# Optimization experiments

Hardware: AMD Instinct MI355X
Metric: run time of the kernel (lower is better)

## Reference

```python
import jax, jax.numpy as jnp
import numpy as np

DIM = 512
N_HEADS = 8
HEAD_DIM = DIM // N_HEADS
TOP_K_RATIO = 0.25
B, L = 2, 2048


def setup_inputs() -> dict:
    key = jax.random.key(0)
    k1, k2, k3, k4, k5 = jax.random.split(key, 5)
    s = 0.02
    return {
        "x": jax.random.normal(k1, (B, L, DIM), jnp.float32),
        "w_qkv": jax.random.normal(k2, (3 * DIM, DIM), jnp.float32) * s,
        "b_qkv": jnp.zeros((3 * DIM,), jnp.float32),
        "w_out": jax.random.normal(k3, (DIM, DIM), jnp.float32) * s,
        "b_out": jnp.zeros((DIM,), jnp.float32),
    }


def reference(x, w_qkv, b_qkv, w_out, b_out):
    Bx, Lx, C = x.shape
    scale = HEAD_DIM ** -0.5
    top_k = max(1, int(TOP_K_RATIO * Lx))

    qkv = x @ w_qkv.T + b_qkv  # [B, L, 3*C]
    qkv = qkv.reshape(Bx, Lx, 3, N_HEADS, HEAD_DIM)
    q, k, v = qkv[:, :, 0], qkv[:, :, 1], qkv[:, :, 2]  # [B, L, H, D]

    scores = jnp.einsum('blhd,bshd->bhls', q, k) * scale  # [B, H, L, L]

    _, top_idx = jax.lax.top_k(scores, top_k)  # [B, H, L, K]
    bi = jnp.arange(Bx)[:, None, None, None]
    hi = jnp.arange(N_HEADS)[None, :, None, None]
    li = jnp.arange(Lx)[None, None, :, None]
    mask = jnp.zeros(scores.shape, bool).at[bi, hi, li, top_idx].set(True)

    masked = jnp.where(mask, scores, -jnp.inf)
    probs = jax.nn.softmax(masked, axis=-1)  # [B, H, L, L]

    out = jnp.einsum('bhls,bshd->blhd', probs, v).reshape(Bx, Lx, C)
    return out @ w_out.T + b_out
```

## Files before the change

kernel.cpp:

```cpp
#include <hip/hip_runtime.h>

#define B_ 2
#define L_ 2048
#define DIM_ 512
#define NH_ 8
#define HD_ 64
#define TOPK_ 512

typedef __attribute__((ext_vector_type(8))) short short8;
typedef __attribute__((ext_vector_type(4))) float f32x4;
typedef unsigned short ushort_t;

__device__ __forceinline__ unsigned f2ord(float f) {
  unsigned u = __float_as_uint(f);
  return (u >> 31) ? ~u : (u | 0x80000000u);
}
__device__ __forceinline__ float ord2f(unsigned k) {
  unsigned u = (k >> 31) ? (k ^ 0x80000000u) : ~k;
  return __uint_as_float(u);
}
__device__ __forceinline__ ushort_t bfrne(float f) {
  unsigned u = __float_as_uint(f);
  return (ushort_t)((u + 0x7FFFu + ((u >> 16) & 1u)) >> 16);
}

__global__ __launch_bounds__(256) void gemm_qkv(
    const float* __restrict__ A, const float* __restrict__ Bw,
    const float* __restrict__ bias,
    ushort_t* __restrict__ Qh, ushort_t* __restrict__ Ql,
    ushort_t* __restrict__ Kh, ushort_t* __restrict__ Kl,
    ushort_t* __restrict__ Vt)
{
  constexpr int BM = 128, BN = 128, BK = 16, TM = 8, TN = 8;
  const int M = B_ * L_, N = 3 * DIM_, K = DIM_;
  __shared__ float As[BK][BM];
  __shared__ float Bs[BK][BN];
  const int tid = threadIdx.x;
  const int m0 = blockIdx.y * BM;
  const int n0 = blockIdx.x * BN;
  constexpr int TX = BN / TN;
  const int tn = (tid % TX) * TN;
  const int tm = (tid / TX) * TM;

  float acc[TM][TN];
#pragma unroll
  for (int i = 0; i < TM; ++i)
#pragma unroll
    for (int j = 0; j < TN; ++j) acc[i][j] = 0.f;

  constexpr int A4 = BM * BK / 4;
  constexpr int B4 = BN * BK / 4;

  for (int k0 = 0; k0 < K; k0 += BK) {
    for (int idx = tid; idx < A4; idx += 256) {
      int e = idx * 4;
      int row = e / BK, col = e % BK;
      float4 v = *(const float4*)(A + (size_t)(m0 + row) * K + k0 + col);
      As[col][row] = v.x; As[col+1][row] = v.y; As[col+2][row] = v.z; As[col+3][row] = v.w;
    }
    for (int idx = tid; idx < B4; idx += 256) {
      int e = idx * 4;
      int row = e / BK, col = e % BK;
      float4 v = *(const float4*)(Bw + (size_t)(n0 + row) * K + k0 + col);
      Bs[col][row] = v.x; Bs[col+1][row] = v.y; Bs[col+2][row] = v.z; Bs[col+3][row] = v.w;
    }
    __syncthreads();
#pragma unroll
    for (int kk = 0; kk < BK; ++kk) {
      float a[TM], b[TN];
#pragma unroll
      for (int i = 0; i < TM; i += 4) *(float4*)&a[i] = *(const float4*)&As[kk][tm + i];
#pragma unroll
      for (int j = 0; j < TN; j += 4) *(float4*)&b[j] = *(const float4*)&Bs[kk][tn + j];
#pragma unroll
      for (int i = 0; i < TM; ++i)
#pragma unroll
        for (int j = 0; j < TN; ++j) acc[i][j] = fmaf(a[i], b[j], acc[i][j]);
    }
    __syncthreads();
  }

#pragma unroll
  for (int i = 0; i < TM; ++i) {
    const int m = m0 + tm + i;
    const int b = m >> 11, l = m & (L_ - 1);
#pragma unroll
    for (int j = 0; j < TN; ++j) {
      const int n = n0 + tn + j;
      float v = acc[i][j] + bias[n];
      const int which = n >> 9, h = (n >> 6) & (NH_ - 1), d = n & (HD_ - 1);
      const int bh = b * NH_ + h;
      if (which == 0) {
        v *= 0.125f;
        ushort_t hi = bfrne(v);
        float hf = __uint_as_float((unsigned)hi << 16);
        ushort_t lo = bfrne(v - hf);
        const size_t o = ((size_t)bh * L_ + l) * HD_ + d;
        Qh[o] = hi; Ql[o] = lo;
      } else if (which == 1) {
        ushort_t hi = bfrne(v);
        float hf = __uint_as_float((unsigned)hi << 16);
        ushort_t lo = bfrne(v - hf);
        const size_t o = ((size_t)bh * L_ + l) * HD_ + d;
        Kh[o] = hi; Kl[o] = lo;
      } else {
        Vt[((size_t)bh * HD_ + d) * L_ + l] = bfrne(v);
      }
    }
  }
}

__global__ __launch_bounds__(256) void gemm_out(
    const float* __restrict__ A, const float* __restrict__ Bw,
    const float* __restrict__ bias, float* __restrict__ out)
{
  constexpr int BM = 64, BN = 64, BK = 16, TM = 4, TN = 4;
  const int N = DIM_, K = DIM_;
  __shared__ float As[BK][BM];
  __shared__ float Bs[BK][BN];
  const int tid = threadIdx.x;
  const int m0 = blockIdx.y * BM;
  const int n0 = blockIdx.x * BN;
  constexpr int TX = BN / TN;
  const int tn = (tid % TX) * TN;
  const int tm = (tid / TX) * TM;

  float acc[TM][TN];
#pragma unroll
  for (int i = 0; i < TM; ++i)
#pragma unroll
    for (int j = 0; j < TN; ++j) acc[i][j] = 0.f;

  constexpr int A4 = BM * BK / 4;
  constexpr int B4 = BN * BK / 4;

  for (int k0 = 0; k0 < K; k0 += BK) {
    for (int idx = tid; idx < A4; idx += 256) {
      int e = idx * 4;
      int row = e / BK, col = e % BK;
      float4 v = *(const float4*)(A + (size_t)(m0 + row) * K + k0 + col);
      As[col][row] = v.x; As[col+1][row] = v.y; As[col+2][row] = v.z; As[col+3][row] = v.w;
    }
    for (int idx = tid; idx < B4; idx += 256) {
      int e = idx * 4;
      int row = e / BK, col = e % BK;
      float4 v = *(const float4*)(Bw + (size_t)(n0 + row) * K + k0 + col);
      Bs[col][row] = v.x; Bs[col+1][row] = v.y; Bs[col+2][row] = v.z; Bs[col+3][row] = v.w;
    }
    __syncthreads();
#pragma unroll
    for (int kk = 0; kk < BK; ++kk) {
      float a[TM], b[TN];
#pragma unroll
      for (int i = 0; i < TM; i += 4) *(float4*)&a[i] = *(const float4*)&As[kk][tm + i];
#pragma unroll
      for (int j = 0; j < TN; j += 4) *(float4*)&b[j] = *(const float4*)&Bs[kk][tn + j];
#pragma unroll
      for (int i = 0; i < TM; ++i)
#pragma unroll
        for (int j = 0; j < TN; ++j) acc[i][j] = fmaf(a[i], b[j], acc[i][j]);
    }
    __syncthreads();
  }

#pragma unroll
  for (int i = 0; i < TM; ++i) {
    const int m = m0 + tm + i;
#pragma unroll
    for (int j = 0; j < TN; ++j)
      out[(size_t)m * N + n0 + tn + j] = acc[i][j] + bias[n0 + tn + j];
  }
}

__global__ __launch_bounds__(256, 4) void sgemm_k(
    const ushort_t* __restrict__ Qh, const ushort_t* __restrict__ Ql,
    const ushort_t* __restrict__ Kh, const ushort_t* __restrict__ Kl,
    float* __restrict__ S, int row0, int CH)
{
  const int lane = threadIdx.x & 63, wid = threadIdx.x >> 6;
  const int bh = blockIdx.z;
  const int m0 = blockIdx.y * 64;
  const int n0 = blockIdx.x * 128 + wid * 32;
  const int arow = lane & 15, agrp = lane >> 4;

  short8 kh[2][2], kl[2][2];
#pragma unroll
  for (int kt = 0; kt < 2; ++kt) {
    const size_t ka = ((size_t)bh * L_ + n0 + kt * 16 + arow) * HD_ + agrp * 8;
    kh[kt][0] = *(const short8*)(Kh + ka);
    kh[kt][1] = *(const short8*)(Kh + ka + 32);
    kl[kt][0] = *(const short8*)(Kl + ka);
    kl[kt][1] = *(const short8*)(Kl + ka + 32);
  }

  float* schunk = S + (size_t)bh * CH * L_;
#pragma unroll
  for (int rt = 0; rt < 4; ++rt) {
    const size_t qa = ((size_t)bh * L_ + row0 + m0 + rt * 16 + arow) * HD_ + agrp * 8;
    const short8 qh0 = *(const short8*)(Qh + qa);
    const short8 qh1 = *(const short8*)(Qh + qa + 32);
    const short8 ql0 = *(const short8*)(Ql + qa);
    const short8 ql1 = *(const short8*)(Ql + qa + 32);
#pragma unroll
    for (int kt = 0; kt < 2; ++kt) {
      f32x4 aA = {0.f, 0.f, 0.f, 0.f}, aB = {0.f, 0.f, 0.f, 0.f};
      aA = __builtin_amdgcn_mfma_f32_16x16x32_bf16(qh0, kh[kt][0], aA, 0, 0, 0);
      aB = __builtin_amdgcn_mfma_f32_16x16x32_bf16(qh1, kh[kt][1], aB, 0, 0, 0);
      aA = __builtin_amdgcn_mfma_f32_16x16x32_bf16(ql0, kh[kt][0], aA, 0, 0, 0);
      aB = __builtin_amdgcn_mfma_f32_16x16x32_bf16(ql1, kh[kt][1], aB, 0, 0, 0);
      aA = __builtin_amdgcn_mfma_f32_16x16x32_bf16(qh0, kl[kt][0], aA, 0, 0, 0);
      aB = __builtin_amdgcn_mfma_f32_16x16x32_bf16(qh1, kl[kt][1], aB, 0, 0, 0);
#pragma unroll
      for (int rr = 0; rr < 4; ++rr)
        schunk[(size_t)(m0 + rt * 16 + agrp * 4 + rr) * L_ + n0 + kt * 16 + arow]
            = aA[rr] + aB[rr];
    }
  }
}

__global__ __launch_bounds__(512, 4) void selpv_k(
    const float* __restrict__ S, const ushort_t* __restrict__ Vt,
    float* __restrict__ AO, int row0, int CH)
{
  __shared__ ushort_t pl[8][2056];
  __shared__ float red[8 * 512];
  __shared__ float invs[8];

  const int tid = threadIdx.x, lane = tid & 63, wid = tid >> 6;
  const int bh = blockIdx.y;
  const int blk = blockIdx.x;
  const int arow = lane & 15, agrp = lane >> 4;

  {
    const float* srow = S + ((size_t)bh * CH + blk * 8 + wid) * L_;
    unsigned keys[32];
    float mx = -3.0e38f;
#pragma unroll
    for (int t = 0; t < 32; ++t) {
      const float s = srow[lane + 64 * t];
      keys[t] = f2ord(s);
      mx = fmaxf(mx, s);
    }
#pragma unroll
    for (int off = 32; off; off >>= 1) mx = fmaxf(mx, __shfl_xor(mx, off));

    unsigned P = 0;
#pragma unroll 1
    for (int bit = 31; bit >= 8; --bit) {
      const unsigned cand = P | (1u << bit);
      int c = 0;
#pragma unroll
      for (int t = 0; t < 32; ++t)
        c += (int)__popcll(__ballot(keys[t] >= cand));
      if (c >= TOPK_) P = cand;
    }

    int base = 0;
    float part = 0.f;
#pragma unroll
    for (int t = 0; t < 32; ++t) {
      const bool sel = keys[t] >= P;
      const unsigned long long mb = __ballot(sel);
      const int pos = base + (int)__popcll(mb & ((1ull << lane) - 1ull));
      const float p = (sel && pos < TOPK_) ? __expf(ord2f(keys[t]) - mx) : 0.f;
      pl[wid][lane + 64 * t] = bfrne(p);
      part += p;
      base += (int)__popcll(mb);
    }
#pragma unroll
    for (int off = 32; off; off >>= 1) part += __shfl_xor(part, off);
    if (lane == 0) invs[wid] = 1.f / part;
  }
  __syncthreads();

  f32x4 o0 = {0.f,0.f,0.f,0.f}, o1 = o0, o2 = o0, o3 = o0;
  {
    const int key00 = wid << 8;
    const size_t vrow = ((size_t)bh * HD_ + arow) * L_;
#pragma unroll 2
    for (int ks = 0; ks < 8; ++ks) {
      const int kb = key00 + ks * 32 + agrp * 8;
      const short8 pa = *(const short8*)&pl[arow & 7][kb];
      const size_t vb0 = vrow + kb;
      const short8 v0 = *(const short8*)(Vt + vb0);
      const short8 v1 = *(const short8*)(Vt + vb0 + 16 * L_);
      const short8 v2 = *(const short8*)(Vt + vb0 + 32 * L_);
      const short8 v3 = *(const short8*)(Vt + vb0 + 48 * L_);
      o0 = __builtin_amdgcn_mfma_f32_16x16x32_bf16(pa, v0, o0, 0, 0, 0);
      o1 = __builtin_amdgcn_mfma_f32_16x16x32_bf16(pa, v1, o1, 0, 0, 0);
      o2 = __builtin_amdgcn_mfma_f32_16x16x32_bf16(pa, v2, o2, 0, 0, 0);
      o3 = __builtin_amdgcn_mfma_f32_16x16x32_bf16(pa, v3, o3, 0, 0, 0);
    }
  }

  if (agrp < 2) {
#pragma unroll
    for (int rr = 0; rr < 4; ++rr) {
      const int row = agrp * 4 + rr;
      red[wid * 512 + row * 64 +  0 + arow] = o0[rr];
      red[wid * 512 + row * 64 + 16 + arow] = o1[rr];
      red[wid * 512 + row * 64 + 32 + arow] = o2[rr];
      red[wid * 512 + row * 64 + 48 + arow] = o3[rr];
    }
  }
  __syncthreads();
  {
    const int b = bh >> 3, h = bh & 7;
    const int r = tid >> 6, d = tid & 63;
    float s = 0.f;
#pragma unroll
    for (int w = 0; w < 8; ++w) s += red[w * 512 + r * 64 + d];
    AO[((size_t)(b * L_ + row0 + blk * 8 + r)) * DIM_ + h * HD_ + d] = s * invs[r];
  }
}

__global__ __launch_bounds__(1024, 1) void attn_fused_k(
    const ushort_t* __restrict__ Qh, const ushort_t* __restrict__ Ql,
    const ushort_t* __restrict__ Kh, const ushort_t* __restrict__ Kl,
    const ushort_t* __restrict__ Vt, float* __restrict__ AO)
{
  __shared__ float sc[16][2052];
  __shared__ float invs[16];

  const int tid = threadIdx.x, lane = tid & 63, wid = tid >> 6;
  const int bh = blockIdx.x >> 7;
  const int l0 = (blockIdx.x & 127) << 4;
  const int arow = lane & 15, agrp = lane >> 4;
  const int key00 = wid << 7;

  const size_t qbase = ((size_t)bh * L_ + l0 + arow) * HD_ + agrp * 8;
  const short8 qh0 = *(const short8*)(Qh + qbase);
  const short8 qh1 = *(const short8*)(Qh + qbase + 32);
  const short8 ql0 = *(const short8*)(Ql + qbase);
  const short8 ql1 = *(const short8*)(Ql + qbase + 32);

  {
#pragma unroll
    for (int t = 0; t < 8; ++t) {
      const int key0 = key00 + t * 16;
      const size_t ka = ((size_t)bh * L_ + key0 + arow) * HD_ + agrp * 8;
      const short8 kh0 = *(const short8*)(Kh + ka);
      const short8 kh1 = *(const short8*)(Kh + ka + 32);
      const short8 kl0 = *(const short8*)(Kl + ka);
      const short8 kl1 = *(const short8*)(Kl + ka + 32);
      f32x4 aA = {0.f, 0.f, 0.f, 0.f}, aB = {0.f, 0.f, 0.f, 0.f};
      aA = __builtin_amdgcn_mfma_f32_16x16x32_bf16(qh0, kh0, aA, 0, 0, 0);
      aB = __builtin_amdgcn_mfma_f32_16x16x32_bf16(qh1, kh1, aB, 0, 0, 0);
      aA = __builtin_amdgcn_mfma_f32_16x16x32_bf16(ql0, kh0, aA, 0, 0, 0);
      aB = __builtin_amdgcn_mfma_f32_16x16x32_bf16(ql1, kh1, aB, 0, 0, 0);
      aA = __builtin_amdgcn_mfma_f32_16x16x32_bf16(qh0, kl0, aA, 0, 0, 0);
      aB = __builtin_amdgcn_mfma_f32_16x16x32_bf16(qh1, kl1, aB, 0, 0, 0);
#pragma unroll
      for (int rr = 0; rr < 4; ++rr)
        sc[agrp * 4 + rr][key0 + arow] = aA[rr] + aB[rr];
    }
  }
  __syncthreads();

  {
    const int r = wid;
    unsigned keys[32];
    float mx = -3.0e38f;
#pragma unroll
    for (int t = 0; t < 32; ++t) {
      const float s = sc[r][lane + 64 * t];
      keys[t] = f2ord(s);
      mx = fmaxf(mx, s);
    }
#pragma unroll
    for (int off = 32; off; off >>= 1) mx = fmaxf(mx, __shfl_xor(mx, off));

    unsigned P = 0;
#pragma unroll 1
    for (int bit = 31; bit >= 8; --bit) {
      const unsigned cand = P | (1u << bit);
      int c = 0;
#pragma unroll
      for (int t = 0; t < 32; ++t)
        c += (int)__popcll(__ballot(keys[t] >= cand));
      if (c >= TOPK_) P = cand;
    }

    int base = 0;
    float part = 0.f;
#pragma unroll
    for (int t = 0; t < 32; ++t) {
      const bool sel = keys[t] >= P;
      const unsigned long long mb = __ballot(sel);
      const int pos = base + (int)__popcll(mb & ((1ull << lane) - 1ull));
      const float p = (sel && pos < TOPK_) ? __expf(ord2f(keys[t]) - mx) : 0.f;
      sc[r][lane + 64 * t] = p;
      part += p;
      base += (int)__popcll(mb);
    }
#pragma unroll
    for (int off = 32; off; off >>= 1) part += __shfl_xor(part, off);
    if (lane == 0) invs[r] = 1.f / part;
  }
  __syncthreads();

  f32x4 o0 = {0.f,0.f,0.f,0.f}, o1 = o0, o2 = o0, o3 = o0;
  {
    const size_t vrow = ((size_t)bh * HD_ + arow) * L_;
#pragma unroll
    for (int ks = 0; ks < 4; ++ks) {
      const int kb = key00 + ks * 32 + agrp * 8;
      float pf[8];
      *(float4*)&pf[0] = *(const float4*)&sc[arow][kb];
      *(float4*)&pf[4] = *(const float4*)&sc[arow][kb + 4];
      short8 pa;
#pragma unroll
      for (int j = 0; j < 8; ++j) pa[j] = (short)bfrne(pf[j]);
      const size_t vb0 = vrow + kb;
      const short8 v0 = *(const short8*)(Vt + vb0);
      const short8 v1 = *(const short8*)(Vt + vb0 + 16 * L_);
      const short8 v2 = *(const short8*)(Vt + vb0 + 32 * L_);
      const short8 v3 = *(const short8*)(Vt + vb0 + 48 * L_);
      o0 = __builtin_amdgcn_mfma_f32_16x16x32_bf16(pa, v0, o0, 0, 0, 0);
      o1 = __builtin_amdgcn_mfma_f32_16x16x32_bf16(pa, v1, o1, 0, 0, 0);
      o2 = __builtin_amdgcn_mfma_f32_16x16x32_bf16(pa, v2, o2, 0, 0, 0);
      o3 = __builtin_amdgcn_mfma_f32_16x16x32_bf16(pa, v3, o3, 0, 0, 0);
    }
  }
  __syncthreads();

  float* red = &sc[0][0];
  {
#pragma unroll
    for (int rr = 0; rr < 4; ++rr) {
      const int row = agrp * 4 + rr;
      red[wid * 1024 + row * 64 +  0 + arow] = o0[rr];
      red[wid * 1024 + row * 64 + 16 + arow] = o1[rr];
      red[wid * 1024 + row * 64 + 32 + arow] = o2[rr];
      red[wid * 1024 + row * 64 + 48 + arow] = o3[rr];
    }
  }
  __syncthreads();
  {
    const int b = bh >> 3, h = bh & 7;
    const int r = tid >> 6, d = tid & 63;
    float s = 0.f;
#pragma unroll
    for (int w = 0; w < 16; ++w) s += red[w * 1024 + tid];
    AO[((size_t)(b * L_ + l0 + r)) * DIM_ + h * HD_ + d] = s * invs[r];
  }
}

extern "C" void kernel_launch(void* const* d_in, const int* in_sizes, int n_in,
                              void* d_out, int out_size, void* d_ws, size_t ws_size,
                              hipStream_t stream) {
  const float* x     = (const float*)d_in[0];
  const float* w_qkv = (const float*)d_in[1];
  const float* b_qkv = (const float*)d_in[2];
  const float* w_out = (const float*)d_in[3];
  const float* b_out = (const float*)d_in[4];
  float* out = (float*)d_out;

  const size_t NE = (size_t)B_ * NH_ * L_ * HD_;
  ushort_t* Qh = (ushort_t*)d_ws;
  ushort_t* Ql = Qh + NE;
  ushort_t* Kh = Ql + NE;
  ushort_t* Kl = Kh + NE;
  ushort_t* Vt = Kl + NE;
  float*    AO = (float*)(Vt + NE);
  float*    S  = AO + (size_t)B_ * L_ * DIM_;
  const int M = B_ * L_;

  const size_t base    = 5 * NE * sizeof(ushort_t) + (size_t)B_ * L_ * DIM_ * sizeof(float);
  const size_t perRowB = (size_t)B_ * NH_ * L_ * sizeof(float);

  int CH = 0;
  const int cands[5] = {2048, 1024, 512, 256, 128};
  for (int i = 0; i < 5; ++i)
    if (base + (size_t)cands[i] * perRowB <= ws_size) { CH = cands[i]; break; }

  gemm_qkv<<<dim3((3 * DIM_) / 128, M / 128), 256, 0, stream>>>(
      x, w_qkv, b_qkv, Qh, Ql, Kh, Kl, Vt);

  if (CH) {
    for (int row0 = 0; row0 < L_; row0 += CH) {
      sgemm_k<<<dim3(L_ / 128, CH / 64, B_ * NH_), 256, 0, stream>>>(
          Qh, Ql, Kh, Kl, S, row0, CH);
      selpv_k<<<dim3(CH / 8, B_ * NH_), 512, 0, stream>>>(S, Vt, AO, row0, CH);
    }
  } else {
    attn_fused_k<<<dim3(B_ * NH_ * (L_ / 16)), 1024, 0, stream>>>(Qh, Ql, Kh, Kl, Vt, AO);
  }

  gemm_out<<<dim3(DIM_ / 64, M / 64), 256, 0, stream>>>(AO, w_out, b_out, out);
}
```

Before: 466.3 us.

## Run QKV and output projections on MFMA with split-bf16 operands

Replaces the two FP32 SIMT tiled GEMMs with a templated MFMA kernel that uses a three-term bf16 hi/lo split to keep accuracy close to FP32. New split kernels convert x, w_qkv and w_out to hi/lo bf16 pairs on every call. The attention kernels now write their output directly as hi/lo bf16. The workspace is rearranged so the score buffer S reuses the x split area. This adds three conversion launches and extra memory traffic, and the new GEMM loads its operands straight from global memory without LDS staging.

```diff
diff --git a/kernel.cpp b/kernel.cpp
--- a/kernel.cpp
+++ b/kernel.cpp
@@ -24,151 +24,109 @@
   return (ushort_t)((u + 0x7FFFu + ((u >> 16) & 1u)) >> 16);
 }
 
-__global__ __launch_bounds__(256) void gemm_qkv(
-    const float* __restrict__ A, const float* __restrict__ Bw,
-    const float* __restrict__ bias,
+__global__ __launch_bounds__(256) void split_k(
+    const float* __restrict__ src, ushort_t* __restrict__ dh,
+    ushort_t* __restrict__ dl, int n8)
+{
+  const int i = blockIdx.x * 256 + threadIdx.x;
+  if (i >= n8) return;
+  const float4 a = ((const float4*)src)[2 * i];
+  const float4 b = ((const float4*)src)[2 * i + 1];
+  float f[8] = {a.x, a.y, a.z, a.w, b.x, b.y, b.z, b.w};
+  short8 h, l;
+#pragma unroll
+  for (int j = 0; j < 8; ++j) {
+    const ushort_t hi = bfrne(f[j]);
+    const float hf = __uint_as_float((unsigned)hi << 16);
+    h[j] = (short)hi;
+    l[j] = (short)bfrne(f[j] - hf);
+  }
+  *(short8*)(dh + 8 * (size_t)i) = h;
+  *(short8*)(dl + 8 * (size_t)i) = l;
+}
+
+template<int EPI>
+__global__ __launch_bounds__(128, 2) void mgemm(
+    const ushort_t* __restrict__ Ah, const ushort_t* __restrict__ Al,
+    const ushort_t* __restrict__ Bh, const ushort_t* __restrict__ Bl,
+    const float* __restrict__ bias, int N, float* __restrict__ out,
     ushort_t* __restrict__ Qh, ushort_t* __restrict__ Ql,
     ushort_t* __restrict__ Kh, ushort_t* __restrict__ Kl,
     ushort_t* __restrict__ Vt)
 {
-  constexpr int BM = 128, BN = 128, BK = 16, TM = 8, TN = 8;
-  const int M = B_ * L_, N = 3 * DIM_, K = DIM_;
-  __shared__ float As[BK][BM];
-  __shared__ float Bs[BK][BN];
-  const int tid = threadIdx.x;
-  const int m0 = blockIdx.y * BM;
-  const int n0 = blockIdx.x * BN;
-  constexpr int TX = BN / TN;
-  const int tn = (tid % TX) * TN;
-  const int tm = (tid / TX) * TM;
-
-  float acc[TM][TN];
-#pragma unroll
-  for (int i = 0; i < TM; ++i)
-#pragma unroll
-    for (int j = 0; j < TN; ++j) acc[i][j] = 0.f;
-
-  constexpr int A4 = BM * BK / 4;
-  constexpr int B4 = BN * BK / 4;
-
-  for (int k0 = 0; k0 < K; k0 += BK) {
-    for (int idx = tid; idx < A4; idx += 256) {
-      int e = idx * 4;
-      int row = e / BK, col = e % BK;
-      float4 v = *(const float4*)(A + (size_t)(m0 + row) * K + k0 + col);
-      As[col][row] = v.x; As[col+1][row] = v.y; As[col+2][row] = v.z; As[col+3][row] = v.w;
-    }
-    for (int idx = tid; idx < B4; idx += 256) {
-      int e = idx * 4;
-      int row = e / BK, col = e % BK;
-      float4 v = *(const float4*)(Bw + (size_t)(n0 + row) * K + k0 + col);
-      Bs[col][row] = v.x; Bs[col+1][row] = v.y; Bs[col+2][row] = v.z; Bs[col+3][row] = v.w;
-    }
-    __syncthreads();
-#pragma unroll
-    for (int kk = 0; kk < BK; ++kk) {
-      float a[TM], b[TN];
-#pragma unroll
-      for (int i = 0; i < TM; i += 4) *(float4*)&a[i] = *(const float4*)&As[kk][tm + i];
-#pragma unroll
-      for (int j = 0; j < TN; j += 4) *(float4*)&b[j] = *(const float4*)&Bs[kk][tn + j];
-#pragma unroll
-      for (int i = 0; i < TM; ++i)
-#pragma unroll
-        for (int j = 0; j < TN; ++j) acc[i][j] = fmaf(a[i], b[j], acc[i][j]);
-    }
-    __syncthreads();
-  }
-
-#pragma unroll
-  for (int i = 0; i < TM; ++i) {
-    const int m = m0 + tm + i;
-    const int b = m >> 11, l = m & (L_ - 1);
-#pragma unroll
-    for (int j = 0; j < TN; ++j) {
-      const int n = n0 + tn + j;
-      float v = acc[i][j] + bias[n];
-      const int which = n >> 9, h = (n >> 6) & (NH_ - 1), d = n & (HD_ - 1);
-      const int bh = b * NH_ + h;
-      if (which == 0) {
-        v *= 0.125f;
-        ushort_t hi = bfrne(v);
-        float hf = __uint_as_float((unsigned)hi << 16);
-        ushort_t lo = bfrne(v - hf);
-        const size_t o = ((size_t)bh * L_ + l) * HD_ + d;
-        Qh[o] = hi; Ql[o] = lo;
-      } else if (which == 1) {
-        ushort_t hi = bfrne(v);
-        float hf = __uint_as_float((unsigned)hi << 16);
-        ushort_t lo = bfrne(v - hf);
-        const size_t o = ((size_t)bh * L_ + l) * HD_ + d;
-        Kh[o] = hi; Kl[o] = lo;
-      } else {
-        Vt[((size_t)bh * HD_ + d) * L_ + l] = bfrne(v);
+  constexpr int K = DIM_;
+  const int lane = threadIdx.x & 63, wid = threadIdx.x >> 6;
+  const int m0 = blockIdx.y * 64;
+  const int n0 = blockIdx.x * 64 + wid * 32;
+  const int arow = lane & 15, agrp = lane >> 4;
+
+  f32x4 acc[4][2];
+#pragma unroll
+  for (int rt = 0; rt < 4; ++rt)
+#pragma unroll
+    for (int ct = 0; ct < 2; ++ct) acc[rt][ct] = (f32x4){0.f, 0.f, 0.f, 0.f};
+
+#pragma unroll 1
+  for (int ks = 0; ks < K / 32; ++ks) {
+    const int ko = ks * 32 + agrp * 8;
+    short8 ah[4], al[4];
+#pragma unroll
+    for (int rt = 0; rt < 4; ++rt) {
+      const size_t ao = (size_t)(m0 + rt * 16 + arow) * K + ko;
+      ah[rt] = *(const short8*)(Ah + ao);
+      al[rt] = *(const short8*)(Al + ao);
+    }
+    short8 bhf[2], blf[2];
+#pragma unroll
+    for (int ct = 0; ct < 2; ++ct) {
+      const size_t bo = (size_t)(n0 + ct * 16 + arow) * K + ko;
+      bhf[ct] = *(const short8*)(Bh + bo);
+      blf[ct] = *(const short8*)(Bl + bo);
+    }
+#pragma unroll
+    for (int rt = 0; rt < 4; ++rt)
+#pragma unroll
+      for (int ct = 0; ct < 2; ++ct) {
+        acc[rt][ct] = __builtin_amdgcn_mfma_f32_16x16x32_bf16(ah[rt], bhf[ct], acc[rt][ct], 0, 0, 0);
+        acc[rt][ct] = __builtin_amdgcn_mfma_f32_16x16x32_bf16(al[rt], bhf[ct], acc[rt][ct], 0, 0, 0);
+        acc[rt][ct] = __builtin_amdgcn_mfma_f32_16x16x32_bf16(ah[rt], blf[ct], acc[rt][ct], 0, 0, 0);
       }
-    }
-  }
-}
-
-__global__ __launch_bounds__(256) void gemm_out(
-    const float* __restrict__ A, const float* __restrict__ Bw,
-    const float* __restrict__ bias, float* __restrict__ out)
-{
-  constexpr int BM = 64, BN = 64, BK = 16, TM = 4, TN = 4;
-  const int N = DIM_, K = DIM_;
-  __shared__ float As[BK][BM];
-  __shared__ float Bs[BK][BN];
-  const int tid = threadIdx.x;
-  const int m0 = blockIdx.y * BM;
-  const int n0 = blockIdx.x * BN;
-  constexpr int TX = BN / TN;
-  const int tn = (tid % TX) * TN;
-  const int tm = (tid / TX) * TM;
-
-  float acc[TM][TN];
-#pragma unroll
-  for (int i = 0; i < TM; ++i)
-#pragma unroll
-    for (int j = 0; j < TN; ++j) acc[i][j] = 0.f;
-
-  constexpr int A4 = BM * BK / 4;
-  constexpr int B4 = BN * BK / 4;
-
-  for (int k0 = 0; k0 < K; k0 += BK) {
-    for (int idx = tid; idx < A4; idx += 256) {
-      int e = idx * 4;
-      int row = e / BK, col = e % BK;
-      float4 v = *(const float4*)(A + (size_t)(m0 + row) * K + k0 + col);
-      As[col][row] = v.x; As[col+1][row] = v.y; As[col+2][row] = v.z; As[col+3][row] = v.w;
-    }
-    for (int idx = tid; idx < B4; idx += 256) {
-      int e = idx * 4;
-      int row = e / BK, col = e % BK;
-      float4 v = *(const float4*)(Bw + (size_t)(n0 + row) * K + k0 + col);
-      Bs[col][row] = v.x; Bs[col+1][row] = v.y; Bs[col+2][row] = v.z; Bs[col+3][row] = v.w;
-    }
-    __syncthreads();
-#pragma unroll
-    for (int kk = 0; kk < BK; ++kk) {
-      float a[TM], b[TN];
-#pragma unroll
-      for (int i = 0; i < TM; i += 4) *(float4*)&a[i] = *(const float4*)&As[kk][tm + i];
-#pragma unroll
-      for (int j = 0; j < TN; j += 4) *(float4*)&b[j] = *(const float4*)&Bs[kk][tn + j];
-#pragma unroll
-      for (int i = 0; i < TM; ++i)
-#pragma unroll
-        for (int j = 0; j < TN; ++j) acc[i][j] = fmaf(a[i], b[j], acc[i][j]);
-    }
-    __syncthreads();
-  }
-
-#pragma unroll
-  for (int i = 0; i < TM; ++i) {
-    const int m = m0 + tm + i;
-#pragma unroll
-    for (int j = 0; j < TN; ++j)
-      out[(size_t)m * N + n0 + tn + j] = acc[i][j] + bias[n0 + tn + j];
+  }
+
+#pragma unroll
+  for (int rt = 0; rt < 4; ++rt) {
+#pragma unroll
+    for (int ct = 0; ct < 2; ++ct) {
+#pragma unroll
+      for (int rr = 0; rr < 4; ++rr) {
+        const int m = m0 + rt * 16 + agrp * 4 + rr;
+        const int n = n0 + ct * 16 + arow;
+        float v = acc[rt][ct][rr] + bias[n];
+        if (EPI == 0) {
+          out[(size_t)m * N + n] = v;
+        } else {
+          const int b = m >> 11, l = m & (L_ - 1);
+          const int which = n >> 9, h = (n >> 6) & (NH_ - 1), d = n & (HD_ - 1);
+          const int bh = b * NH_ + h;
+          if (which == 0) {
+            v *= 0.125f;
+            ushort_t hi = bfrne(v);
+            float hf = __uint_as_float((unsigned)hi << 16);
+            ushort_t lo = bfrne(v - hf);
+            const size_t o = ((size_t)bh * L_ + l) * HD_ + d;
+            Qh[o] = hi; Ql[o] = lo;
+          } else if (which == 1) {
+            ushort_t hi = bfrne(v);
+            float hf = __uint_as_float((unsigned)hi << 16);
+            ushort_t lo = bfrne(v - hf);
+            const size_t o = ((size_t)bh * L_ + l) * HD_ + d;
+            Kh[o] = hi; Kl[o] = lo;
+          } else {
+            Vt[((size_t)bh * HD_ + d) * L_ + l] = bfrne(v);
+          }
+        }
+      }
+    }
   }
 }
 
@@ -220,7 +178,7 @@
 
 __global__ __launch_bounds__(512, 4) void selpv_k(
     const float* __restrict__ S, const ushort_t* __restrict__ Vt,
-    float* __restrict__ AO, int row0, int CH)
+    ushort_t* __restrict__ AOh, ushort_t* __restrict__ AOl, int row0, int CH)
 {
   __shared__ ushort_t pl[8][2056];
   __shared__ float red[8 * 512];
@@ -310,14 +268,20 @@
     float s = 0.f;
 #pragma unroll
     for (int w = 0; w < 8; ++w) s += red[w * 512 + r * 64 + d];
-    AO[((size_t)(b * L_ + row0 + blk * 8 + r)) * DIM_ + h * HD_ + d] = s * invs[r];
+    const float sv = s * invs[r];
+    const ushort_t hi = bfrne(sv);
+    const float hf = __uint_as_float((unsigned)hi << 16);
+    const size_t oidx = ((size_t)(b * L_ + row0 + blk * 8 + r)) * DIM_ + h * HD_ + d;
+    AOh[oidx] = hi;
+    AOl[oidx] = bfrne(sv - hf);
   }
 }
 
 __global__ __launch_bounds__(1024, 1) void attn_fused_k(
     const ushort_t* __restrict__ Qh, const ushort_t* __restrict__ Ql,
     const ushort_t* __restrict__ Kh, const ushort_t* __restrict__ Kl,
-    const ushort_t* __restrict__ Vt, float* __restrict__ AO)
+    const ushort_t* __restrict__ Vt,
+    ushort_t* __restrict__ AOh, ushort_t* __restrict__ AOl)
 {
   __shared__ float sc[16][2052];
   __shared__ float invs[16];
@@ -442,7 +406,12 @@
     float s = 0.f;
 #pragma unroll
     for (int w = 0; w < 16; ++w) s += red[w * 1024 + tid];
-    AO[((size_t)(b * L_ + l0 + r)) * DIM_ + h * HD_ + d] = s * invs[r];
+    const float sv = s * invs[r];
+    const ushort_t hi = bfrne(sv);
+    const float hf = __uint_as_float((unsigned)hi << 16);
+    const size_t oidx = ((size_t)(b * L_ + l0 + r)) * DIM_ + h * HD_ + d;
+    AOh[oidx] = hi;
+    AOl[oidx] = bfrne(sv - hf);
   }
 }
 
@@ -456,36 +425,52 @@
   const float* b_out = (const float*)d_in[4];
   float* out = (float*)d_out;
 
-  const size_t NE = (size_t)B_ * NH_ * L_ * HD_;
-  ushort_t* Qh = (ushort_t*)d_ws;
-  ushort_t* Ql = Qh + NE;
-  ushort_t* Kh = Ql + NE;
-  ushort_t* Kl = Kh + NE;
-  ushort_t* Vt = Kl + NE;
-  float*    AO = (float*)(Vt + NE);
-  float*    S  = AO + (size_t)B_ * L_ * DIM_;
-  const int M = B_ * L_;
-
-  const size_t base    = 5 * NE * sizeof(ushort_t) + (size_t)B_ * L_ * DIM_ * sizeof(float);
+  const size_t NE  = (size_t)B_ * NH_ * L_ * HD_;
+  const size_t NWQ = (size_t)3 * DIM_ * DIM_;
+  const size_t NWO = (size_t)DIM_ * DIM_;
+
+  ushort_t* us  = (ushort_t*)d_ws;
+  ushort_t* Qh  = us;
+  ushort_t* Ql  = Qh + NE;
+  ushort_t* Kh  = Ql + NE;
+  ushort_t* Kl  = Kh + NE;
+  ushort_t* Vt  = Kl + NE;
+  ushort_t* AOh = Vt + NE;
+  ushort_t* AOl = AOh + NE;
+  ushort_t* woh = AOl + NE;
+  ushort_t* wol = woh + NWO;
+  ushort_t* xh  = wol + NWO;
+  ushort_t* xl  = xh + NE;
+  ushort_t* wqh = xl + NE;
+  ushort_t* wql = wqh + NWQ;
+  float*    S   = (float*)xh;
+
+  const size_t sOffB   = (size_t)(7 * NE + 2 * NWO) * sizeof(ushort_t);
   const size_t perRowB = (size_t)B_ * NH_ * L_ * sizeof(float);
 
   int CH = 0;
-  const int cands[5] = {2048, 1024, 512, 256, 128};
-  for (int i = 0; i < 5; ++i)
-    if (base + (size_t)cands[i] * perRowB <= ws_size) { CH = cands[i]; break; }
-
-  gemm_qkv<<<dim3((3 * DIM_) / 128, M / 128), 256, 0, stream>>>(
-      x, w_qkv, b_qkv, Qh, Ql, Kh, Kl, Vt);
+  const int cands[6] = {2048, 1024, 512, 256, 128, 64};
+  for (int i = 0; i < 6; ++i)
+    if (sOffB + (size_t)cands[i] * perRowB <= ws_size) { CH = cands[i]; break; }
+
+  split_k<<<(int)((NE  / 8 + 255) / 256), 256, 0, stream>>>(x,     xh,  xl,  (int)(NE  / 8));
+  split_k<<<(int)((NWQ / 8 + 255) / 256), 256, 0, stream>>>(w_qkv, wqh, wql, (int)(NWQ / 8));
+  split_k<<<(int)((NWO / 8 + 255) / 256), 256, 0, stream>>>(w_out, woh, wol, (int)(NWO / 8));
+
+  mgemm<1><<<dim3((3 * DIM_) / 64, (B_ * L_) / 64), 128, 0, stream>>>(
+      xh, xl, wqh, wql, b_qkv, 3 * DIM_, nullptr, Qh, Ql, Kh, Kl, Vt);
 
   if (CH) {
     for (int row0 = 0; row0 < L_; row0 += CH) {
       sgemm_k<<<dim3(L_ / 128, CH / 64, B_ * NH_), 256, 0, stream>>>(
           Qh, Ql, Kh, Kl, S, row0, CH);
-      selpv_k<<<dim3(CH / 8, B_ * NH_), 512, 0, stream>>>(S, Vt, AO, row0, CH);
+      selpv_k<<<dim3(CH / 8, B_ * NH_), 512, 0, stream>>>(S, Vt, AOh, AOl, row0, CH);
     }
   } else {
-    attn_fused_k<<<dim3(B_ * NH_ * (L_ / 16)), 1024, 0, stream>>>(Qh, Ql, Kh, Kl, Vt, AO);
-  }
-
-  gemm_out<<<dim3(DIM_ / 64, M / 64), 256, 0, stream>>>(AO, w_out, b_out, out);
-}
+    attn_fused_k<<<dim3(B_ * NH_ * (L_ / 16)), 1024, 0, stream>>>(
+        Qh, Ql, Kh, Kl, Vt, AOh, AOl);
+  }
+
+  mgemm<0><<<dim3(DIM_ / 64, (B_ * L_) / 64), 128, 0, stream>>>(
+      AOh, AOl, woh, wol, b_out, DIM_, out, nullptr, nullptr, nullptr, nullptr, nullptr);
+}
```

Measured after the change: 414.7 us. -11.1%, faster.
